# Performance work log

Hardware: AMD Instinct MI355X
Metric: run time of the kernel (lower is better)

## Reference

```python
import jax, jax.numpy as jnp
import numpy as np

CTX = 1024   # context_window
D = 512      # emb_dim
B = 8        # batch


def make_rotary_matrix(ctx, d):
    """Dense block-diagonal RoPE rotation matrices R: [ctx, d, d]."""
    pos = jnp.arange(ctx, dtype=jnp.float32)[:, None]          # [ctx, 1]
    i = jnp.arange(d // 2, dtype=jnp.float32)                  # [d/2]
    theta = pos / (10000.0 ** (2.0 * i / d))                   # [ctx, d/2]
    cos, sin = jnp.cos(theta), jnp.sin(theta)
    idx = jnp.arange(d // 2)
    R = jnp.zeros((ctx, d, d), jnp.float32)
    R = R.at[:, 2 * idx, 2 * idx].set(cos)
    R = R.at[:, 2 * idx, 2 * idx + 1].set(-sin)
    R = R.at[:, 2 * idx + 1, 2 * idx].set(sin)
    R = R.at[:, 2 * idx + 1, 2 * idx + 1].set(cos)
    return R


def setup_inputs() -> dict:
    key = jax.random.key(0)
    ks = jax.random.split(key, 8)
    s = 1.0 / np.sqrt(D)
    inp = {
        "x": jax.random.normal(ks[0], (B, CTX, D), jnp.float32),
        "w_q": jax.random.uniform(ks[1], (D, D), jnp.float32, -s, s),
        "b_q": jax.random.uniform(ks[2], (D,), jnp.float32, -s, s),
        "w_k": jax.random.uniform(ks[3], (D, D), jnp.float32, -s, s),
        "b_k": jax.random.uniform(ks[4], (D,), jnp.float32, -s, s),
        "w_v": jax.random.uniform(ks[5], (D, D), jnp.float32, -s, s),
        "b_v": jax.random.uniform(ks[6], (D,), jnp.float32, -s, s),
        "R": make_rotary_matrix(CTX, D),
        "kv_cache": 0,  # bool flag; does not affect output
    }
    return inp


def reference(x, w_q, b_q, w_k, b_k, w_v, b_v, R, kv_cache):
    B_, C, Dm = x.shape
    q = x @ w_q.T + b_q                      # [B, C, D]
    k = x @ w_k.T + b_k
    v = x @ w_v.T + b_v
    Rc = R[:C]                               # [C, D, D]
    # torch.bmm(q.transpose(0,1), R.transpose(1,2)).transpose(0,1)
    # out[b,c,e] = sum_d q[b,c,d] * R[c,e,d]
    q_rot = jnp.einsum("bcd,ced->bce", q, Rc)
    k_rot = jnp.einsum("bcd,ced->bce", k, Rc)
    # causal SDPA (eval mode: dropout omitted)
    scale = 1.0 / jnp.sqrt(jnp.asarray(Dm, jnp.float32))
    scores = jnp.einsum("bqe,bke->bqk", q_rot, k_rot) * scale   # [B, C, C]
    causal = jnp.tril(jnp.ones((C, C), bool))
    scores = jnp.where(causal, scores, jnp.finfo(scores.dtype).min)
    attn = jax.nn.softmax(scores, axis=-1)
    return jnp.einsum("bqk,bkd->bqd", attn, v)
```

## Files before the change

kernel.cpp:

```cpp
#include <hip/hip_runtime.h>

#define BATCH 8
#define CTXN  1024
#define DMODEL 512

using short8  = __attribute__((ext_vector_type(8))) short;
using f32x16  = __attribute__((ext_vector_type(16))) float;

typedef const void __attribute__((address_space(1)))* as1_cvp;
typedef void __attribute__((address_space(3)))* as3_vp;

__device__ __forceinline__ unsigned short f2bf(float f) {
  unsigned int u = __float_as_uint(f);
  u += 0x7fffu + ((u >> 16) & 1u);
  return (unsigned short)(u >> 16);
}
__device__ __forceinline__ float bf2f(unsigned short u) {
  return __uint_as_float((unsigned int)u << 16);
}

#define X4  1048576
#define W4  65536
#define CAST_BLOCKS 4864
__global__ __launch_bounds__(256) void prep_all(const float* __restrict__ x,
                                                const float* __restrict__ wq,
                                                const float* __restrict__ wk,
                                                const float* __restrict__ wv,
                                                unsigned short* __restrict__ xb,
                                                unsigned short* __restrict__ wb,
                                                float2* __restrict__ tab) {
  if (blockIdx.x < CAST_BLOCKS) {
    int gid = blockIdx.x * 256 + threadIdx.x;
    const float4* src; ushort4* dst;
    if (gid < X4)                { src = (const float4*)x  + gid;              dst = (ushort4*)xb + gid; }
    else if (gid < X4 + W4)      { int o = gid - X4;        src = (const float4*)wq + o; dst = (ushort4*)wb + o; }
    else if (gid < X4 + 2 * W4)  { int o = gid - X4 - W4;   src = (const float4*)wk + o; dst = (ushort4*)(wb + 262144) + o; }
    else                         { int o = gid - X4 - 2*W4; src = (const float4*)wv + o; dst = (ushort4*)(wb + 524288) + o; }
    float4 f = *src;
    ushort4 u;
    u.x = f2bf(f.x); u.y = f2bf(f.y); u.z = f2bf(f.z); u.w = f2bf(f.w);
    *dst = u;
  } else {
    int c = blockIdx.x - CAST_BLOCKS;
    int i = threadIdx.x;
    float freq = exp2f((float)i * (-13.287712379549449f / 256.0f));
    float th = (float)c * freq;
    float sn, cs;
    sincosf(th, &sn, &cs);
    tab[c * 256 + i] = make_float2(cs, sn);
  }
}


__device__ __forceinline__ void issue_tile(const unsigned short* __restrict__ gA, int ldA,
                                           const unsigned short* __restrict__ gB, int ldB,
                                           unsigned short* sA, unsigned short* sB,
                                           int slot, int tid) {
  unsigned short* dA = sA + (slot << 13);
  unsigned short* dB = sB + (slot << 13);
#pragma unroll
  for (int c = 0; c < 2; ++c) {
    int li  = (c << 9) + tid;
    int row = li >> 3;
    int ch  = (li & 7) ^ (row & 7);
    __builtin_amdgcn_global_load_lds((as1_cvp)(gA + (size_t)row * ldA + (ch << 3)),
                                     (as3_vp)(dA + (li << 3)), 16, 0, 0);
  }
#pragma unroll
  for (int c = 0; c < 2; ++c) {
    int li  = (c << 9) + tid;
    int row = li >> 3;
    int ch  = (li & 7) ^ (row & 7);
    __builtin_amdgcn_global_load_lds((as1_cvp)(gB + (size_t)row * ldB + (ch << 3)),
                                     (as3_vp)(dB + (li << 3)), 16, 0, 0);
  }
}

__device__ __forceinline__ void gemm_pipe(const unsigned short* __restrict__ gA, int ldA,
                                          const unsigned short* __restrict__ gB, int ldB,
                                          int nt, unsigned short* sA, unsigned short* sB,
                                          int tid, f32x16 acc[2]) {
  const int l = tid & 63, w = tid >> 6, wr = w >> 2, wc = w & 3;
  const int cl = l & 31, hi = l >> 5;
  int aoff[2][4], boff[4];
#pragma unroll
  for (int m = 0; m < 2; ++m) {
    int ra = wr * 64 + m * 32 + cl;
#pragma unroll
    for (int ks = 0; ks < 4; ++ks) {
      int kc = ks * 2 + hi;
      aoff[m][ks] = ra * 64 + ((kc ^ (ra & 7)) << 3);
    }
  }
  {
    int rb = wc * 32 + cl;
#pragma unroll
    for (int ks = 0; ks < 4; ++ks) {
      int kc = ks * 2 + hi;
      boff[ks] = rb * 64 + ((kc ^ (rb & 7)) << 3);
    }
  }
  issue_tile(gA, ldA, gB, ldB, sA, sB, 0, tid);
  issue_tile(gA + 64, ldA, gB + 64, ldB, sA, sB, 1, tid);
  asm volatile("s_waitcnt vmcnt(4)" ::: "memory");
  __builtin_amdgcn_s_barrier();
  __builtin_amdgcn_sched_barrier(0);

  for (int t = 0; t < nt; ++t) {
    const unsigned short* sAb = sA + ((t & 1) << 13);
    const unsigned short* sBb = sB + ((t & 1) << 13);
    short8 af[2][4], bfv[4];
    af[0][0] = *(const short8*)(sAb + aoff[0][0]);
    af[1][0] = *(const short8*)(sAb + aoff[1][0]);
    bfv[0]   = *(const short8*)(sBb + boff[0]);
#pragma unroll
    for (int ks = 0; ks < 3; ++ks) {
      af[0][ks + 1] = *(const short8*)(sAb + aoff[0][ks + 1]);
      af[1][ks + 1] = *(const short8*)(sAb + aoff[1][ks + 1]);
      bfv[ks + 1]   = *(const short8*)(sBb + boff[ks + 1]);
      asm volatile("s_waitcnt lgkmcnt(3)" ::: "memory");
      __builtin_amdgcn_sched_barrier(0);
      __builtin_amdgcn_s_setprio(1);
      acc[0] = __builtin_amdgcn_mfma_f32_32x32x16_bf16(af[0][ks], bfv[ks], acc[0], 0, 0, 0);
      acc[1] = __builtin_amdgcn_mfma_f32_32x32x16_bf16(af[1][ks], bfv[ks], acc[1], 0, 0, 0);
      __builtin_amdgcn_s_setprio(0);
    }
    asm volatile("s_waitcnt lgkmcnt(0)" ::: "memory");
    __builtin_amdgcn_sched_barrier(0);
    __builtin_amdgcn_s_barrier();
    if (t + 2 < nt) {
      issue_tile(gA + (size_t)(t + 2) * 64, ldA, gB + (size_t)(t + 2) * 64, ldB, sA, sB, t & 1, tid);
      asm volatile("s_waitcnt vmcnt(4)" ::: "memory");
    } else {
      asm volatile("s_waitcnt vmcnt(0)" ::: "memory");
    }
    __builtin_amdgcn_sched_barrier(0);
    __builtin_amdgcn_s_setprio(1);
    acc[0] = __builtin_amdgcn_mfma_f32_32x32x16_bf16(af[0][3], bfv[3], acc[0], 0, 0, 0);
    acc[1] = __builtin_amdgcn_mfma_f32_32x32x16_bf16(af[1][3], bfv[3], acc[1], 0, 0, 0);
    __builtin_amdgcn_s_setprio(0);
    __builtin_amdgcn_s_barrier();
    __builtin_amdgcn_sched_barrier(0);
  }
}


__global__ __launch_bounds__(512, 4) void qkv_kernel(const unsigned short* __restrict__ xb,
                                                     const unsigned short* __restrict__ wb,
                                                     const float* __restrict__ bq,
                                                     const float* __restrict__ bk,
                                                     const float* __restrict__ bv,
                                                     const float2* __restrict__ tab,
                                                     unsigned short* __restrict__ qrot,
                                                     unsigned short* __restrict__ krot,
                                                     unsigned short* __restrict__ vt) {
  __shared__ __align__(16) unsigned short sA[2 * 8192];
  __shared__ __align__(16) unsigned short sB[2 * 8192];
  int t = threadIdx.x, w = t >> 6, l = t & 63, wr = w >> 2, wc = w & 3;
  int cl = l & 31, hi = l >> 5;
  int m0 = blockIdx.x * 128, n0 = blockIdx.y * 128;
  f32x16 acc[2] = {};
  gemm_pipe(xb + (size_t)m0 * 512, 512, wb + (size_t)n0 * 512, 512, 8, sA, sB, t, acc);

  int sec = n0 >> 9;
  const float* bias = (sec == 0) ? bq : (sec == 1) ? bk : bv;
  unsigned short* qk_dst = (sec == 0) ? qrot : krot;
  int e = (n0 + wc * 32 + cl) & 511;
  float bsv = bias[e];
  if (sec < 2) {
    int i2 = e >> 1;
#pragma unroll
    for (int m = 0; m < 2; ++m) {
      int rowb = m0 + wr * 64 + m * 32 + 4 * hi;
#pragma unroll
      for (int r = 0; r < 16; ++r) {
        int mg = rowb + (r & 3) + 8 * (r >> 2);
        int cpos = mg & (CTXN - 1);
        float val  = acc[m][r] + bsv;
        float part = __shfl_xor(val, 1);
        float2 cs  = tab[cpos * 256 + i2];
        float o = (e & 1) ? fmaf(part, cs.y, val * cs.x)
                          : fmaf(-part, cs.y, val * cs.x);
        qk_dst[(size_t)mg * 512 + e] = f2bf(o);
      }
    }
  } else {
#pragma unroll
    for (int m = 0; m < 2; ++m) {
      int rowb0 = m0 + wr * 64 + m * 32 + 4 * hi;
#pragma unroll
      for (int q = 0; q < 4; ++q) {
        int rowb = rowb0 + 8 * q;
        int bidx = rowb >> 10;
        int cpos = rowb & (CTXN - 1);
        ushort4 pk;
        pk.x = f2bf(acc[m][q * 4 + 0] + bsv);
        pk.y = f2bf(acc[m][q * 4 + 1] + bsv);
        pk.z = f2bf(acc[m][q * 4 + 2] + bsv);
        pk.w = f2bf(acc[m][q * 4 + 3] + bsv);
        *(ushort4*)(vt + ((size_t)bidx * 512 + e) * 1024 + cpos) = pk;
      }
    }
  }
}

__device__ const unsigned char TRI_IT[36] = {0,1,1,2,2,2,3,3,3,3,4,4,4,4,4,5,5,5,5,5,5,
                                             6,6,6,6,6,6,6,7,7,7,7,7,7,7,7};
__device__ const unsigned char TRI_JT[36] = {0,0,1,0,1,2,0,1,2,3,0,1,2,3,4,0,1,2,3,4,5,
                                             0,1,2,3,4,5,6,0,1,2,3,4,5,6,7};

__global__ __launch_bounds__(512, 4) void scores_kernel(const unsigned short* __restrict__ qr,
                                                        const unsigned short* __restrict__ kr,
                                                        unsigned short* __restrict__ S) {
  int it = TRI_IT[blockIdx.x], jt = TRI_JT[blockIdx.x], b = blockIdx.y;
  __shared__ __align__(16) unsigned short sA[2 * 8192];
  __shared__ __align__(16) unsigned short sB[2 * 8192];
  int t = threadIdx.x, w = t >> 6, l = t & 63, wr = w >> 2, wc = w & 3;
  int cl = l & 31, hi = l >> 5;
  const unsigned short* A  = qr + ((size_t)b << 19) + (size_t)it * 128 * 512;
  const unsigned short* Bp = kr + ((size_t)b << 19) + (size_t)jt * 128 * 512;
  f32x16 acc[2] = {};
  gemm_pipe(A, 512, Bp, 512, 8, sA, sB, t, acc);

  const float scale = 0.04419417382415922f;
  unsigned short* Sb = S + ((size_t)b << 20);
  int j = jt * 128 + wc * 32 + cl;
#pragma unroll
  for (int m = 0; m < 2; ++m) {
    int iqb = it * 128 + wr * 64 + m * 32 + 4 * hi;
#pragma unroll
    for (int r = 0; r < 16; ++r)
      Sb[(size_t)(iqb + (r & 3) + 8 * (r >> 2)) * 1024 + j] = f2bf(acc[m][r] * scale);
  }
}

__global__ __launch_bounds__(256) void softmax_kernel(const unsigned short* __restrict__ S,
                                                      unsigned short* __restrict__ P) {
  int w = threadIdx.x >> 6, l = threadIdx.x & 63;
  int i = blockIdx.x * 4 + w;
  int b = blockIdx.y;
  const unsigned short* row = S + ((size_t)b << 20) + (size_t)i * 1024;
  unsigned short* prow = P + ((size_t)b << 20) + (size_t)i * 1024;
  int len  = i + 1;
  int jmax = ((i >> 7) + 1) << 7;
  float v[16];
  float mx = -3.4e38f;
#pragma unroll
  for (int c = 0; c < 2; ++c) {
    short8 raw = *(const short8*)(row + c * 512 + l * 8);
#pragma unroll
    for (int jj = 0; jj < 8; ++jj) {
      int j = c * 512 + l * 8 + jj;
      float f = bf2f((unsigned short)raw[jj]);
      v[c * 8 + jj] = (j < len) ? f : -3.4e38f;
      mx = fmaxf(mx, v[c * 8 + jj]);
    }
  }
#pragma unroll
  for (int o = 32; o > 0; o >>= 1) mx = fmaxf(mx, __shfl_xor(mx, o));
  float sm = 0.0f;
#pragma unroll
  for (int p = 0; p < 16; ++p) {
    int j = (p >> 3) * 512 + l * 8 + (p & 7);
    v[p] = (j < len) ? __expf(v[p] - mx) : 0.0f;
    sm += v[p];
  }
#pragma unroll
  for (int o = 32; o > 0; o >>= 1) sm += __shfl_xor(sm, o);
  float inv = 1.0f / sm;
#pragma unroll
  for (int c = 0; c < 2; ++c) {
    int jbase = c * 512 + l * 8;
    if (jbase < jmax) {
      short8 outv;
#pragma unroll
      for (int jj = 0; jj < 8; ++jj) outv[jj] = (short)f2bf(v[c * 8 + jj] * inv);
      *(short8*)(prow + jbase) = outv;
    }
  }
}

__global__ __launch_bounds__(512, 4) void pv_kernel(const unsigned short* __restrict__ P,
                                                    const unsigned short* __restrict__ vt,
                                                    float* __restrict__ out) {
  int it = blockIdx.x, nt2 = blockIdx.y, b = blockIdx.z;
  __shared__ __align__(16) unsigned short sA[2 * 8192];
  __shared__ __align__(16) unsigned short sB[2 * 8192];
  int t = threadIdx.x, w = t >> 6, l = t & 63, wr = w >> 2, wc = w & 3;
  int cl = l & 31, hi = l >> 5;
  const unsigned short* A  = P  + ((size_t)b << 20) + (size_t)it * 128 * 1024;
  const unsigned short* Bp = vt + ((size_t)b << 19) + (size_t)nt2 * 128 * 1024;
  int nt = (it + 1) * 2;
  f32x16 acc[2] = {};
  gemm_pipe(A, 1024, Bp, 1024, nt, sA, sB, t, acc);

  float* ob = out + ((size_t)b << 19);
  int d = nt2 * 128 + wc * 32 + cl;
#pragma unroll
  for (int m = 0; m < 2; ++m) {
    int iqb = it * 128 + wr * 64 + m * 32 + 4 * hi;
#pragma unroll
    for (int r = 0; r < 16; ++r)
      ob[(size_t)(iqb + (r & 3) + 8 * (r >> 2)) * 512 + d] = acc[m][r];
  }
}

extern "C" void kernel_launch(void* const* d_in, const int* in_sizes, int n_in,
                              void* d_out, int out_size, void* d_ws, size_t ws_size,
                              hipStream_t stream) {
  const float* x  = (const float*)d_in[0];
  const float* wq = (const float*)d_in[1];
  const float* bq = (const float*)d_in[2];
  const float* wk = (const float*)d_in[3];
  const float* bk = (const float*)d_in[4];
  const float* wv = (const float*)d_in[5];
  const float* bv = (const float*)d_in[6];
  float* out = (float*)d_out;

  char* ws = (char*)d_ws;
  float2*         tab  = (float2*)(ws);
  unsigned short* xb   = (unsigned short*)(ws + (2ull  << 20));
  unsigned short* wb   = (unsigned short*)(ws + (10ull << 20));
  unsigned short* qrot = (unsigned short*)(ws + (12ull << 20));
  unsigned short* krot = (unsigned short*)(ws + (20ull << 20));
  unsigned short* vt   = (unsigned short*)(ws + (28ull << 20));
  unsigned short* S    = (unsigned short*)(ws + (36ull << 20));
  unsigned short* P    = (unsigned short*)(ws + (52ull << 20));

  prep_all<<<dim3(CAST_BLOCKS + CTXN), dim3(256), 0, stream>>>(x, wq, wk, wv, xb, wb, tab);
  qkv_kernel<<<dim3(64, 12), dim3(512), 0, stream>>>(xb, wb, bq, bk, bv, tab, qrot, krot, vt);
  scores_kernel<<<dim3(36, BATCH), dim3(512), 0, stream>>>(qrot, krot, S);
  softmax_kernel<<<dim3(256, BATCH), dim3(256), 0, stream>>>(S, P);
  pv_kernel<<<dim3(8, 4, BATCH), dim3(512), 0, stream>>>(P, vt, out);
}
```

Baseline: 77.15 us.

## Fuse scores, softmax and PV into a single flash-attention kernel

Replaces the three-kernel attention path (scores to global S, softmax to global P, then PV GEMM) with one flash-style kernel. Each 512-thread block owns 32 query rows of one batch and walks KV tiles of 256 with an online softmax: row max and sum are reduced across waves through shared memory, and P is staged in LDS as bf16. The goal is to drop the S and P round trips through HBM and two kernel launches. In exchange it reads Q, K and V fragments straight from global memory with no LDS tiling, uses small 32-row tiles across 256 blocks with uneven causal work, and adds three barriers per KV tile.

```diff
diff --git a/kernel.cpp b/kernel.cpp
--- a/kernel.cpp
+++ b/kernel.cpp
@@ -14,9 +14,6 @@
   unsigned int u = __float_as_uint(f);
   u += 0x7fffu + ((u >> 16) & 1u);
   return (unsigned short)(u >> 16);
-}
-__device__ __forceinline__ float bf2f(unsigned short u) {
-  return __uint_as_float((unsigned int)u << 16);
 }
 
 #define X4  1048576
@@ -51,7 +48,6 @@
   }
 }
 
-
 __device__ __forceinline__ void issue_tile(const unsigned short* __restrict__ gA, int ldA,
                                            const unsigned short* __restrict__ gB, int ldB,
                                            unsigned short* sA, unsigned short* sB,
@@ -204,104 +200,113 @@
   }
 }
 
-__device__ const unsigned char TRI_IT[36] = {0,1,1,2,2,2,3,3,3,3,4,4,4,4,4,5,5,5,5,5,5,
-                                             6,6,6,6,6,6,6,7,7,7,7,7,7,7,7};
-__device__ const unsigned char TRI_JT[36] = {0,0,1,0,1,2,0,1,2,3,0,1,2,3,4,0,1,2,3,4,5,
-                                             0,1,2,3,4,5,6,0,1,2,3,4,5,6,7};
-
-__global__ __launch_bounds__(512, 4) void scores_kernel(const unsigned short* __restrict__ qr,
-                                                        const unsigned short* __restrict__ kr,
-                                                        unsigned short* __restrict__ S) {
-  int it = TRI_IT[blockIdx.x], jt = TRI_JT[blockIdx.x], b = blockIdx.y;
-  __shared__ __align__(16) unsigned short sA[2 * 8192];
-  __shared__ __align__(16) unsigned short sB[2 * 8192];
-  int t = threadIdx.x, w = t >> 6, l = t & 63, wr = w >> 2, wc = w & 3;
-  int cl = l & 31, hi = l >> 5;
-  const unsigned short* A  = qr + ((size_t)b << 19) + (size_t)it * 128 * 512;
-  const unsigned short* Bp = kr + ((size_t)b << 19) + (size_t)jt * 128 * 512;
-  f32x16 acc[2] = {};
-  gemm_pipe(A, 512, Bp, 512, 8, sA, sB, t, acc);
+#define KVB 256
+#define PPITCH 264
+
+__global__ __launch_bounds__(512, 2) void fattn_kernel(const unsigned short* __restrict__ qrot,
+                                                       const unsigned short* __restrict__ krot,
+                                                       const unsigned short* __restrict__ vt,
+                                                       float* __restrict__ out) {
+  int wgid = blockIdx.x;
+  int s = wgid >> 3, b = wgid & 7;
+  int iq0 = s * 32;
+  int kvmax = iq0 + 32;
+  int njt = (kvmax + KVB - 1) / KVB;
+
+  const unsigned short* Qb = qrot + ((size_t)b << 19) + (size_t)iq0 * 512;
+  const unsigned short* Kb = krot + ((size_t)b << 19);
+  const unsigned short* Vb = vt   + ((size_t)b << 19);
+
+  __shared__ __align__(16) unsigned short Ps[32 * PPITCH];
+  __shared__ float redM[32][8];
+  __shared__ float redS[32][8];
+
+  int t = threadIdx.x, w = t >> 6, l = t & 63, cl = l & 31, hi = l >> 5;
+
+  f32x16 O0 = {}, O1 = {};
+  float m_run[16], l_run[16];
+#pragma unroll
+  for (int rr = 0; rr < 16; ++rr) { m_run[rr] = -3.0e38f; l_run[rr] = 0.0f; }
 
   const float scale = 0.04419417382415922f;
-  unsigned short* Sb = S + ((size_t)b << 20);
-  int j = jt * 128 + wc * 32 + cl;
-#pragma unroll
-  for (int m = 0; m < 2; ++m) {
-    int iqb = it * 128 + wr * 64 + m * 32 + 4 * hi;
-#pragma unroll
-    for (int r = 0; r < 16; ++r)
-      Sb[(size_t)(iqb + (r & 3) + 8 * (r >> 2)) * 1024 + j] = f2bf(acc[m][r] * scale);
-  }
-}
-
-__global__ __launch_bounds__(256) void softmax_kernel(const unsigned short* __restrict__ S,
-                                                      unsigned short* __restrict__ P) {
-  int w = threadIdx.x >> 6, l = threadIdx.x & 63;
-  int i = blockIdx.x * 4 + w;
-  int b = blockIdx.y;
-  const unsigned short* row = S + ((size_t)b << 20) + (size_t)i * 1024;
-  unsigned short* prow = P + ((size_t)b << 20) + (size_t)i * 1024;
-  int len  = i + 1;
-  int jmax = ((i >> 7) + 1) << 7;
-  float v[16];
-  float mx = -3.4e38f;
-#pragma unroll
-  for (int c = 0; c < 2; ++c) {
-    short8 raw = *(const short8*)(row + c * 512 + l * 8);
-#pragma unroll
-    for (int jj = 0; jj < 8; ++jj) {
-      int j = c * 512 + l * 8 + jj;
-      float f = bf2f((unsigned short)raw[jj]);
-      v[c * 8 + jj] = (j < len) ? f : -3.4e38f;
-      mx = fmaxf(mx, v[c * 8 + jj]);
-    }
-  }
-#pragma unroll
-  for (int o = 32; o > 0; o >>= 1) mx = fmaxf(mx, __shfl_xor(mx, o));
-  float sm = 0.0f;
-#pragma unroll
-  for (int p = 0; p < 16; ++p) {
-    int j = (p >> 3) * 512 + l * 8 + (p & 7);
-    v[p] = (j < len) ? __expf(v[p] - mx) : 0.0f;
-    sm += v[p];
-  }
-#pragma unroll
-  for (int o = 32; o > 0; o >>= 1) sm += __shfl_xor(sm, o);
-  float inv = 1.0f / sm;
-#pragma unroll
-  for (int c = 0; c < 2; ++c) {
-    int jbase = c * 512 + l * 8;
-    if (jbase < jmax) {
-      short8 outv;
-#pragma unroll
-      for (int jj = 0; jj < 8; ++jj) outv[jj] = (short)f2bf(v[c * 8 + jj] * inv);
-      *(short8*)(prow + jbase) = outv;
-    }
-  }
-}
-
-__global__ __launch_bounds__(512, 4) void pv_kernel(const unsigned short* __restrict__ P,
-                                                    const unsigned short* __restrict__ vt,
-                                                    float* __restrict__ out) {
-  int it = blockIdx.x, nt2 = blockIdx.y, b = blockIdx.z;
-  __shared__ __align__(16) unsigned short sA[2 * 8192];
-  __shared__ __align__(16) unsigned short sB[2 * 8192];
-  int t = threadIdx.x, w = t >> 6, l = t & 63, wr = w >> 2, wc = w & 3;
-  int cl = l & 31, hi = l >> 5;
-  const unsigned short* A  = P  + ((size_t)b << 20) + (size_t)it * 128 * 1024;
-  const unsigned short* Bp = vt + ((size_t)b << 19) + (size_t)nt2 * 128 * 1024;
-  int nt = (it + 1) * 2;
-  f32x16 acc[2] = {};
-  gemm_pipe(A, 1024, Bp, 1024, nt, sA, sB, t, acc);
-
-  float* ob = out + ((size_t)b << 19);
-  int d = nt2 * 128 + wc * 32 + cl;
-#pragma unroll
-  for (int m = 0; m < 2; ++m) {
-    int iqb = it * 128 + wr * 64 + m * 32 + 4 * hi;
-#pragma unroll
-    for (int r = 0; r < 16; ++r)
-      ob[(size_t)(iqb + (r & 3) + 8 * (r >> 2)) * 512 + d] = acc[m][r];
+
+  for (int jt = 0; jt < njt; ++jt) {
+    int j0 = jt * KVB + w * 32;
+    bool act = (j0 < kvmax);
+    f32x16 aE = {}, aO = {};
+    if (act) {
+      const unsigned short* Kw = Kb + (size_t)j0 * 512;
+#pragma unroll
+      for (int ks = 0; ks < 32; ++ks) {
+        short8 qa = *(const short8*)(Qb + (size_t)cl * 512 + ks * 16 + hi * 8);
+        short8 kf = *(const short8*)(Kw + (size_t)cl * 512 + ks * 16 + hi * 8);
+        if (ks & 1) aO = __builtin_amdgcn_mfma_f32_32x32x16_bf16(qa, kf, aO, 0, 0, 0);
+        else        aE = __builtin_amdgcn_mfma_f32_32x32x16_bf16(qa, kf, aE, 0, 0, 0);
+      }
+    }
+    int jcol = j0 + cl;
+    float sv[16];
+#pragma unroll
+    for (int rr = 0; rr < 16; ++rr) {
+      int rowi = iq0 + (rr & 3) + 8 * (rr >> 2) + 4 * hi;
+      float xv = (aE[rr] + aO[rr]) * scale;
+      sv[rr] = (act && jcol <= rowi) ? xv : -3.0e38f;
+    }
+#pragma unroll
+    for (int rr = 0; rr < 16; ++rr) {
+      float m = sv[rr];
+#pragma unroll
+      for (int o = 16; o > 0; o >>= 1) m = fmaxf(m, __shfl_xor(m, o));
+      if (cl == 0) redM[(rr & 3) + 8 * (rr >> 2) + 4 * hi][w] = m;
+    }
+    __syncthreads();
+    float sc[16];
+#pragma unroll
+    for (int rr = 0; rr < 16; ++rr) {
+      int row = (rr & 3) + 8 * (rr >> 2) + 4 * hi;
+      float4 a = *(const float4*)&redM[row][0];
+      float4 bq = *(const float4*)&redM[row][4];
+      float tm = fmaxf(fmaxf(fmaxf(a.x, a.y), fmaxf(a.z, a.w)),
+                       fmaxf(fmaxf(bq.x, bq.y), fmaxf(bq.z, bq.w)));
+      float nm = fmaxf(m_run[rr], tm);
+      sc[rr] = __expf(m_run[rr] - nm);
+      m_run[rr] = nm;
+      float p = __expf(sv[rr] - nm);
+      sv[rr] = p;
+      float sp = p;
+#pragma unroll
+      for (int o = 16; o > 0; o >>= 1) sp += __shfl_xor(sp, o);
+      if (cl == 0) redS[row][w] = sp;
+      Ps[row * PPITCH + w * 32 + cl] = f2bf(p);
+      O0[rr] *= sc[rr];
+      O1[rr] *= sc[rr];
+    }
+    __syncthreads();
+#pragma unroll
+    for (int rr = 0; rr < 16; ++rr) {
+      int row = (rr & 3) + 8 * (rr >> 2) + 4 * hi;
+      float4 a = *(const float4*)&redS[row][0];
+      float4 bq = *(const float4*)&redS[row][4];
+      l_run[rr] = l_run[rr] * sc[rr] + (a.x + a.y + a.z + a.w + bq.x + bq.y + bq.z + bq.w);
+    }
+    int kkmax = min(16, (kvmax - jt * KVB + 15) >> 4);
+    const unsigned short* Vw = Vb + (size_t)(w * 64) * 1024 + jt * KVB;
+    for (int kk = 0; kk < kkmax; ++kk) {
+      short8 pa = *(const short8*)(Ps + cl * PPITCH + kk * 16 + hi * 8);
+      short8 v0 = *(const short8*)(Vw + (size_t)cl * 1024 + kk * 16 + hi * 8);
+      short8 v1 = *(const short8*)(Vw + (size_t)(cl + 32) * 1024 + kk * 16 + hi * 8);
+      O0 = __builtin_amdgcn_mfma_f32_32x32x16_bf16(pa, v0, O0, 0, 0, 0);
+      O1 = __builtin_amdgcn_mfma_f32_32x32x16_bf16(pa, v1, O1, 0, 0, 0);
+    }
+    __syncthreads();
+  }
+  float* ob = out + ((size_t)b << 19) + (size_t)iq0 * 512;
+#pragma unroll
+  for (int rr = 0; rr < 16; ++rr) {
+    int row = (rr & 3) + 8 * (rr >> 2) + 4 * hi;
+    float inv = 1.0f / l_run[rr];
+    ob[(size_t)row * 512 + w * 64 + cl]      = O0[rr] * inv;
+    ob[(size_t)row * 512 + w * 64 + 32 + cl] = O1[rr] * inv;
   }
 }
 
@@ -324,12 +329,8 @@
   unsigned short* qrot = (unsigned short*)(ws + (12ull << 20));
   unsigned short* krot = (unsigned short*)(ws + (20ull << 20));
   unsigned short* vt   = (unsigned short*)(ws + (28ull << 20));
-  unsigned short* S    = (unsigned short*)(ws + (36ull << 20));
-  unsigned short* P    = (unsigned short*)(ws + (52ull << 20));
 
   prep_all<<<dim3(CAST_BLOCKS + CTXN), dim3(256), 0, stream>>>(x, wq, wk, wv, xb, wb, tab);
   qkv_kernel<<<dim3(64, 12), dim3(512), 0, stream>>>(xb, wb, bq, bk, bv, tab, qrot, krot, vt);
-  scores_kernel<<<dim3(36, BATCH), dim3(512), 0, stream>>>(qrot, krot, S);
-  softmax_kernel<<<dim3(256, BATCH), dim3(256), 0, stream>>>(S, P);
-  pv_kernel<<<dim3(8, 4, BATCH), dim3(512), 0, stream>>>(P, vt, out);
-}
+  fattn_kernel<<<dim3(256), dim3(512), 0, stream>>>(qrot, krot, vt, out);
+}
```

Result: slower. 153.5 us (+99.0%).

## Use 64-row query tiles with 256-thread blocks for scores and PV GEMMs

Applied to the files above, without the earlier changes.

Adds a 64x128 tile GEMM pipeline (gemm_pipe64) with 4 warps and switches the scores and PV kernels to it. Causal triangle enumeration becomes finer (72 tiles per batch instead of 36), and PV blocks for 64-row query tiles stop at the 128-column boundary. The aim is more blocks for better CU occupancy and load balance, and less wasted causal work. The cost is lower per-block reuse of the B operand and more global loads per unit of work.

```diff
diff --git a/kernel.cpp b/kernel.cpp
--- a/kernel.cpp
+++ b/kernel.cpp
@@ -51,7 +51,6 @@
   }
 }
 
-
 __device__ __forceinline__ void issue_tile(const unsigned short* __restrict__ gA, int ldA,
                                            const unsigned short* __restrict__ gB, int ldB,
                                            unsigned short* sA, unsigned short* sB,
@@ -131,6 +130,98 @@
     if (t + 2 < nt) {
       issue_tile(gA + (size_t)(t + 2) * 64, ldA, gB + (size_t)(t + 2) * 64, ldB, sA, sB, t & 1, tid);
       asm volatile("s_waitcnt vmcnt(4)" ::: "memory");
+    } else {
+      asm volatile("s_waitcnt vmcnt(0)" ::: "memory");
+    }
+    __builtin_amdgcn_sched_barrier(0);
+    __builtin_amdgcn_s_setprio(1);
+    acc[0] = __builtin_amdgcn_mfma_f32_32x32x16_bf16(af[0][3], bfv[3], acc[0], 0, 0, 0);
+    acc[1] = __builtin_amdgcn_mfma_f32_32x32x16_bf16(af[1][3], bfv[3], acc[1], 0, 0, 0);
+    __builtin_amdgcn_s_setprio(0);
+    __builtin_amdgcn_s_barrier();
+    __builtin_amdgcn_sched_barrier(0);
+  }
+}
+
+__device__ __forceinline__ void issue_tile64(const unsigned short* __restrict__ gA, int ldA,
+                                             const unsigned short* __restrict__ gB, int ldB,
+                                             unsigned short* sA, unsigned short* sB,
+                                             int slot, int tid) {
+  unsigned short* dA = sA + (slot << 12);
+  unsigned short* dB = sB + (slot << 13);
+#pragma unroll
+  for (int c = 0; c < 2; ++c) {
+    int li  = (c << 8) + tid;
+    int row = li >> 3;
+    int ch  = (li & 7) ^ (row & 7);
+    __builtin_amdgcn_global_load_lds((as1_cvp)(gA + (size_t)row * ldA + (ch << 3)),
+                                     (as3_vp)(dA + (li << 3)), 16, 0, 0);
+  }
+#pragma unroll
+  for (int c = 0; c < 4; ++c) {
+    int li  = (c << 8) + tid;
+    int row = li >> 3;
+    int ch  = (li & 7) ^ (row & 7);
+    __builtin_amdgcn_global_load_lds((as1_cvp)(gB + (size_t)row * ldB + (ch << 3)),
+                                     (as3_vp)(dB + (li << 3)), 16, 0, 0);
+  }
+}
+
+__device__ __forceinline__ void gemm_pipe64(const unsigned short* __restrict__ gA, int ldA,
+                                            const unsigned short* __restrict__ gB, int ldB,
+                                            int nt, unsigned short* sA, unsigned short* sB,
+                                            int tid, f32x16 acc[2]) {
+  const int l = tid & 63, w = tid >> 6;
+  const int cl = l & 31, hi = l >> 5;
+  int aoff[2][4], boff[4];
+#pragma unroll
+  for (int m = 0; m < 2; ++m) {
+    int ra = m * 32 + cl;
+#pragma unroll
+    for (int ks = 0; ks < 4; ++ks) {
+      int kc = ks * 2 + hi;
+      aoff[m][ks] = ra * 64 + ((kc ^ (ra & 7)) << 3);
+    }
+  }
+  {
+    int rb = w * 32 + cl;
+#pragma unroll
+    for (int ks = 0; ks < 4; ++ks) {
+      int kc = ks * 2 + hi;
+      boff[ks] = rb * 64 + ((kc ^ (rb & 7)) << 3);
+    }
+  }
+  issue_tile64(gA, ldA, gB, ldB, sA, sB, 0, tid);
+  issue_tile64(gA + 64, ldA, gB + 64, ldB, sA, sB, 1, tid);
+  asm volatile("s_waitcnt vmcnt(6)" ::: "memory");
+  __builtin_amdgcn_s_barrier();
+  __builtin_amdgcn_sched_barrier(0);
+
+  for (int t = 0; t < nt; ++t) {
+    const unsigned short* sAb = sA + ((t & 1) << 12);
+    const unsigned short* sBb = sB + ((t & 1) << 13);
+    short8 af[2][4], bfv[4];
+    af[0][0] = *(const short8*)(sAb + aoff[0][0]);
+    af[1][0] = *(const short8*)(sAb + aoff[1][0]);
+    bfv[0]   = *(const short8*)(sBb + boff[0]);
+#pragma unroll
+    for (int ks = 0; ks < 3; ++ks) {
+      af[0][ks + 1] = *(const short8*)(sAb + aoff[0][ks + 1]);
+      af[1][ks + 1] = *(const short8*)(sAb + aoff[1][ks + 1]);
+      bfv[ks + 1]   = *(const short8*)(sBb + boff[ks + 1]);
+      asm volatile("s_waitcnt lgkmcnt(3)" ::: "memory");
+      __builtin_amdgcn_sched_barrier(0);
+      __builtin_amdgcn_s_setprio(1);
+      acc[0] = __builtin_amdgcn_mfma_f32_32x32x16_bf16(af[0][ks], bfv[ks], acc[0], 0, 0, 0);
+      acc[1] = __builtin_amdgcn_mfma_f32_32x32x16_bf16(af[1][ks], bfv[ks], acc[1], 0, 0, 0);
+      __builtin_amdgcn_s_setprio(0);
+    }
+    asm volatile("s_waitcnt lgkmcnt(0)" ::: "memory");
+    __builtin_amdgcn_sched_barrier(0);
+    __builtin_amdgcn_s_barrier();
+    if (t + 2 < nt) {
+      issue_tile64(gA + (size_t)(t + 2) * 64, ldA, gB + (size_t)(t + 2) * 64, ldB, sA, sB, t & 1, tid);
+      asm volatile("s_waitcnt vmcnt(6)" ::: "memory");
     } else {
       asm volatile("s_waitcnt vmcnt(0)" ::: "memory");
     }
@@ -204,30 +295,36 @@
   }
 }
 
-__device__ const unsigned char TRI_IT[36] = {0,1,1,2,2,2,3,3,3,3,4,4,4,4,4,5,5,5,5,5,5,
-                                             6,6,6,6,6,6,6,7,7,7,7,7,7,7,7};
-__device__ const unsigned char TRI_JT[36] = {0,0,1,0,1,2,0,1,2,3,0,1,2,3,4,0,1,2,3,4,5,
-                                             0,1,2,3,4,5,6,0,1,2,3,4,5,6,7};
-
-__global__ __launch_bounds__(512, 4) void scores_kernel(const unsigned short* __restrict__ qr,
+__device__ const unsigned char T64_IT[72] = {
+  0,1,2,2,3,3,4,4,4,5,5,5,6,6,6,6,7,7,7,7,
+  8,8,8,8,8,9,9,9,9,9,10,10,10,10,10,10,11,11,11,11,11,11,
+  12,12,12,12,12,12,12,13,13,13,13,13,13,13,
+  14,14,14,14,14,14,14,14,15,15,15,15,15,15,15,15};
+__device__ const unsigned char T64_JT[72] = {
+  0,0,0,1,0,1,0,1,2,0,1,2,0,1,2,3,0,1,2,3,
+  0,1,2,3,4,0,1,2,3,4,0,1,2,3,4,5,0,1,2,3,4,5,
+  0,1,2,3,4,5,6,0,1,2,3,4,5,6,
+  0,1,2,3,4,5,6,7,0,1,2,3,4,5,6,7};
+
+__global__ __launch_bounds__(256, 3) void scores_kernel(const unsigned short* __restrict__ qr,
                                                         const unsigned short* __restrict__ kr,
                                                         unsigned short* __restrict__ S) {
-  int it = TRI_IT[blockIdx.x], jt = TRI_JT[blockIdx.x], b = blockIdx.y;
-  __shared__ __align__(16) unsigned short sA[2 * 8192];
+  int it = T64_IT[blockIdx.x], jt = T64_JT[blockIdx.x], b = blockIdx.y;
+  __shared__ __align__(16) unsigned short sA[2 * 4096];
   __shared__ __align__(16) unsigned short sB[2 * 8192];
-  int t = threadIdx.x, w = t >> 6, l = t & 63, wr = w >> 2, wc = w & 3;
+  int t = threadIdx.x, w = t >> 6, l = t & 63;
   int cl = l & 31, hi = l >> 5;
-  const unsigned short* A  = qr + ((size_t)b << 19) + (size_t)it * 128 * 512;
+  const unsigned short* A  = qr + ((size_t)b << 19) + (size_t)it * 64 * 512;
   const unsigned short* Bp = kr + ((size_t)b << 19) + (size_t)jt * 128 * 512;
   f32x16 acc[2] = {};
-  gemm_pipe(A, 512, Bp, 512, 8, sA, sB, t, acc);
+  gemm_pipe64(A, 512, Bp, 512, 8, sA, sB, t, acc);
 
   const float scale = 0.04419417382415922f;
   unsigned short* Sb = S + ((size_t)b << 20);
-  int j = jt * 128 + wc * 32 + cl;
+  int j = jt * 128 + w * 32 + cl;
 #pragma unroll
   for (int m = 0; m < 2; ++m) {
-    int iqb = it * 128 + wr * 64 + m * 32 + 4 * hi;
+    int iqb = it * 64 + m * 32 + 4 * hi;
 #pragma unroll
     for (int r = 0; r < 16; ++r)
       Sb[(size_t)(iqb + (r & 3) + 8 * (r >> 2)) * 1024 + j] = f2bf(acc[m][r] * scale);
@@ -280,25 +377,25 @@
   }
 }
 
-__global__ __launch_bounds__(512, 4) void pv_kernel(const unsigned short* __restrict__ P,
+__global__ __launch_bounds__(256, 3) void pv_kernel(const unsigned short* __restrict__ P,
                                                     const unsigned short* __restrict__ vt,
                                                     float* __restrict__ out) {
   int it = blockIdx.x, nt2 = blockIdx.y, b = blockIdx.z;
-  __shared__ __align__(16) unsigned short sA[2 * 8192];
+  __shared__ __align__(16) unsigned short sA[2 * 4096];
   __shared__ __align__(16) unsigned short sB[2 * 8192];
-  int t = threadIdx.x, w = t >> 6, l = t & 63, wr = w >> 2, wc = w & 3;
+  int t = threadIdx.x, w = t >> 6, l = t & 63;
   int cl = l & 31, hi = l >> 5;
-  const unsigned short* A  = P  + ((size_t)b << 20) + (size_t)it * 128 * 1024;
+  const unsigned short* A  = P  + ((size_t)b << 20) + (size_t)it * 64 * 1024;
   const unsigned short* Bp = vt + ((size_t)b << 19) + (size_t)nt2 * 128 * 1024;
-  int nt = (it + 1) * 2;
+  int nt = ((it >> 1) + 1) * 2;
   f32x16 acc[2] = {};
-  gemm_pipe(A, 1024, Bp, 1024, nt, sA, sB, t, acc);
+  gemm_pipe64(A, 1024, Bp, 1024, nt, sA, sB, t, acc);
 
   float* ob = out + ((size_t)b << 19);
-  int d = nt2 * 128 + wc * 32 + cl;
+  int d = nt2 * 128 + w * 32 + cl;
 #pragma unroll
   for (int m = 0; m < 2; ++m) {
-    int iqb = it * 128 + wr * 64 + m * 32 + 4 * hi;
+    int iqb = it * 64 + m * 32 + 4 * hi;
 #pragma unroll
     for (int r = 0; r < 16; ++r)
       ob[(size_t)(iqb + (r & 3) + 8 * (r >> 2)) * 512 + d] = acc[m][r];
@@ -329,7 +426,7 @@
 
   prep_all<<<dim3(CAST_BLOCKS + CTXN), dim3(256), 0, stream>>>(x, wq, wk, wv, xb, wb, tab);
   qkv_kernel<<<dim3(64, 12), dim3(512), 0, stream>>>(xb, wb, bq, bk, bv, tab, qrot, krot, vt);
-  scores_kernel<<<dim3(36, BATCH), dim3(512), 0, stream>>>(qrot, krot, S);
+  scores_kernel<<<dim3(72, BATCH), dim3(256), 0, stream>>>(qrot, krot, S);
   softmax_kernel<<<dim3(256, BATCH), dim3(256), 0, stream>>>(S, P);
-  pv_kernel<<<dim3(8, 4, BATCH), dim3(512), 0, stream>>>(P, vt, out);
-}
+  pv_kernel<<<dim3(16, 4, BATCH), dim3(256), 0, stream>>>(P, vt, out);
+}
```

Result: faster. 73.88 us (-4.2%).

## Shrink GEMM tiles to 64x128 with 256-thread blocks for more parallelism

Applied to the files above, without the earlier changes.

Replaces the 128x128 GEMM tile, run by 512 threads in 8 waves, with a 64x128 tile run by 256 threads in 4 waves. The QKV, scores and PV kernels all switch to the smaller tile. The scores triangle is re-enumerated at finer granularity (72 tiles), and PV's causal K-extent is recomputed per 64-row tile. The aim is to raise block count and occupancy and to cut wasted causal work, trading away some B-tile reuse per block and adding extra loads and barriers.

```diff
diff --git a/kernel.cpp b/kernel.cpp
--- a/kernel.cpp
+++ b/kernel.cpp
@@ -51,24 +51,23 @@
   }
 }
 
-
-__device__ __forceinline__ void issue_tile(const unsigned short* __restrict__ gA, int ldA,
-                                           const unsigned short* __restrict__ gB, int ldB,
-                                           unsigned short* sA, unsigned short* sB,
-                                           int slot, int tid) {
-  unsigned short* dA = sA + (slot << 13);
+__device__ __forceinline__ void issue_tile64(const unsigned short* __restrict__ gA, int ldA,
+                                             const unsigned short* __restrict__ gB, int ldB,
+                                             unsigned short* sA, unsigned short* sB,
+                                             int slot, int tid) {
+  unsigned short* dA = sA + (slot << 12);
   unsigned short* dB = sB + (slot << 13);
 #pragma unroll
   for (int c = 0; c < 2; ++c) {
-    int li  = (c << 9) + tid;
+    int li  = (c << 8) + tid;
     int row = li >> 3;
     int ch  = (li & 7) ^ (row & 7);
     __builtin_amdgcn_global_load_lds((as1_cvp)(gA + (size_t)row * ldA + (ch << 3)),
                                      (as3_vp)(dA + (li << 3)), 16, 0, 0);
   }
 #pragma unroll
-  for (int c = 0; c < 2; ++c) {
-    int li  = (c << 9) + tid;
+  for (int c = 0; c < 4; ++c) {
+    int li  = (c << 8) + tid;
     int row = li >> 3;
     int ch  = (li & 7) ^ (row & 7);
     __builtin_amdgcn_global_load_lds((as1_cvp)(gB + (size_t)row * ldB + (ch << 3)),
@@ -76,16 +75,16 @@
   }
 }
 
-__device__ __forceinline__ void gemm_pipe(const unsigned short* __restrict__ gA, int ldA,
-                                          const unsigned short* __restrict__ gB, int ldB,
-                                          int nt, unsigned short* sA, unsigned short* sB,
-                                          int tid, f32x16 acc[2]) {
-  const int l = tid & 63, w = tid >> 6, wr = w >> 2, wc = w & 3;
+__device__ __forceinline__ void gemm_pipe64(const unsigned short* __restrict__ gA, int ldA,
+                                            const unsigned short* __restrict__ gB, int ldB,
+                                            int nt, unsigned short* sA, unsigned short* sB,
+                                            int tid, f32x16 acc[2]) {
+  const int l = tid & 63, w = tid >> 6;
   const int cl = l & 31, hi = l >> 5;
   int aoff[2][4], boff[4];
 #pragma unroll
   for (int m = 0; m < 2; ++m) {
-    int ra = wr * 64 + m * 32 + cl;
+    int ra = m * 32 + cl;
 #pragma unroll
     for (int ks = 0; ks < 4; ++ks) {
       int kc = ks * 2 + hi;
@@ -93,21 +92,21 @@
     }
   }
   {
-    int rb = wc * 32 + cl;
+    int rb = w * 32 + cl;
 #pragma unroll
     for (int ks = 0; ks < 4; ++ks) {
       int kc = ks * 2 + hi;
       boff[ks] = rb * 64 + ((kc ^ (rb & 7)) << 3);
     }
   }
-  issue_tile(gA, ldA, gB, ldB, sA, sB, 0, tid);
-  issue_tile(gA + 64, ldA, gB + 64, ldB, sA, sB, 1, tid);
-  asm volatile("s_waitcnt vmcnt(4)" ::: "memory");
+  issue_tile64(gA, ldA, gB, ldB, sA, sB, 0, tid);
+  issue_tile64(gA + 64, ldA, gB + 64, ldB, sA, sB, 1, tid);
+  asm volatile("s_waitcnt vmcnt(6)" ::: "memory");
   __builtin_amdgcn_s_barrier();
   __builtin_amdgcn_sched_barrier(0);
 
   for (int t = 0; t < nt; ++t) {
-    const unsigned short* sAb = sA + ((t & 1) << 13);
+    const unsigned short* sAb = sA + ((t & 1) << 12);
     const unsigned short* sBb = sB + ((t & 1) << 13);
     short8 af[2][4], bfv[4];
     af[0][0] = *(const short8*)(sAb + aoff[0][0]);
@@ -129,8 +128,8 @@
     __builtin_amdgcn_sched_barrier(0);
     __builtin_amdgcn_s_barrier();
     if (t + 2 < nt) {
-      issue_tile(gA + (size_t)(t + 2) * 64, ldA, gB + (size_t)(t + 2) * 64, ldB, sA, sB, t & 1, tid);
-      asm volatile("s_waitcnt vmcnt(4)" ::: "memory");
+      issue_tile64(gA + (size_t)(t + 2) * 64, ldA, gB + (size_t)(t + 2) * 64, ldB, sA, sB, t & 1, tid);
+      asm volatile("s_waitcnt vmcnt(6)" ::: "memory");
     } else {
       asm volatile("s_waitcnt vmcnt(0)" ::: "memory");
     }
@@ -145,7 +144,7 @@
 }
 
 
-__global__ __launch_bounds__(512, 4) void qkv_kernel(const unsigned short* __restrict__ xb,
+__global__ __launch_bounds__(256, 3) void qkv_kernel(const unsigned short* __restrict__ xb,
                                                      const unsigned short* __restrict__ wb,
                                                      const float* __restrict__ bq,
                                                      const float* __restrict__ bk,
@@ -154,24 +153,24 @@
                                                      unsigned short* __restrict__ qrot,
                                                      unsigned short* __restrict__ krot,
                                                      unsigned short* __restrict__ vt) {
-  __shared__ __align__(16) unsigned short sA[2 * 8192];
+  __shared__ __align__(16) unsigned short sA[2 * 4096];
   __shared__ __align__(16) unsigned short sB[2 * 8192];
-  int t = threadIdx.x, w = t >> 6, l = t & 63, wr = w >> 2, wc = w & 3;
+  int t = threadIdx.x, w = t >> 6, l = t & 63;
   int cl = l & 31, hi = l >> 5;
-  int m0 = blockIdx.x * 128, n0 = blockIdx.y * 128;
+  int m0 = blockIdx.x * 64, n0 = blockIdx.y * 128;
   f32x16 acc[2] = {};
-  gemm_pipe(xb + (size_t)m0 * 512, 512, wb + (size_t)n0 * 512, 512, 8, sA, sB, t, acc);
+  gemm_pipe64(xb + (size_t)m0 * 512, 512, wb + (size_t)n0 * 512, 512, 8, sA, sB, t, acc);
 
   int sec = n0 >> 9;
   const float* bias = (sec == 0) ? bq : (sec == 1) ? bk : bv;
   unsigned short* qk_dst = (sec == 0) ? qrot : krot;
-  int e = (n0 + wc * 32 + cl) & 511;
+  int e = (n0 + w * 32 + cl) & 511;
   float bsv = bias[e];
   if (sec < 2) {
     int i2 = e >> 1;
 #pragma unroll
     for (int m = 0; m < 2; ++m) {
-      int rowb = m0 + wr * 64 + m * 32 + 4 * hi;
+      int rowb = m0 + m * 32 + 4 * hi;
 #pragma unroll
       for (int r = 0; r < 16; ++r) {
         int mg = rowb + (r & 3) + 8 * (r >> 2);
@@ -187,7 +186,7 @@
   } else {
 #pragma unroll
     for (int m = 0; m < 2; ++m) {
-      int rowb0 = m0 + wr * 64 + m * 32 + 4 * hi;
+      int rowb0 = m0 + m * 32 + 4 * hi;
 #pragma unroll
       for (int q = 0; q < 4; ++q) {
         int rowb = rowb0 + 8 * q;
@@ -204,30 +203,36 @@
   }
 }
 
-__device__ const unsigned char TRI_IT[36] = {0,1,1,2,2,2,3,3,3,3,4,4,4,4,4,5,5,5,5,5,5,
-                                             6,6,6,6,6,6,6,7,7,7,7,7,7,7,7};
-__device__ const unsigned char TRI_JT[36] = {0,0,1,0,1,2,0,1,2,3,0,1,2,3,4,0,1,2,3,4,5,
-                                             0,1,2,3,4,5,6,0,1,2,3,4,5,6,7};
-
-__global__ __launch_bounds__(512, 4) void scores_kernel(const unsigned short* __restrict__ qr,
+__device__ const unsigned char T64_IT[72] = {
+  0,1,2,2,3,3,4,4,4,5,5,5,6,6,6,6,7,7,7,7,
+  8,8,8,8,8,9,9,9,9,9,10,10,10,10,10,10,11,11,11,11,11,11,
+  12,12,12,12,12,12,12,13,13,13,13,13,13,13,
+  14,14,14,14,14,14,14,14,15,15,15,15,15,15,15,15};
+__device__ const unsigned char T64_JT[72] = {
+  0,0,0,1,0,1,0,1,2,0,1,2,0,1,2,3,0,1,2,3,
+  0,1,2,3,4,0,1,2,3,4,0,1,2,3,4,5,0,1,2,3,4,5,
+  0,1,2,3,4,5,6,0,1,2,3,4,5,6,
+  0,1,2,3,4,5,6,7,0,1,2,3,4,5,6,7};
+
+__global__ __launch_bounds__(256, 3) void scores_kernel(const unsigned short* __restrict__ qr,
                                                         const unsigned short* __restrict__ kr,
                                                         unsigned short* __restrict__ S) {
-  int it = TRI_IT[blockIdx.x], jt = TRI_JT[blockIdx.x], b = blockIdx.y;
-  __shared__ __align__(16) unsigned short sA[2 * 8192];
+  int it = T64_IT[blockIdx.x], jt = T64_JT[blockIdx.x], b = blockIdx.y;
+  __shared__ __align__(16) unsigned short sA[2 * 4096];
   __shared__ __align__(16) unsigned short sB[2 * 8192];
-  int t = threadIdx.x, w = t >> 6, l = t & 63, wr = w >> 2, wc = w & 3;
+  int t = threadIdx.x, w = t >> 6, l = t & 63;
   int cl = l & 31, hi = l >> 5;
-  const unsigned short* A  = qr + ((size_t)b << 19) + (size_t)it * 128 * 512;
+  const unsigned short* A  = qr + ((size_t)b << 19) + (size_t)it * 64 * 512;
   const unsigned short* Bp = kr + ((size_t)b << 19) + (size_t)jt * 128 * 512;
   f32x16 acc[2] = {};
-  gemm_pipe(A, 512, Bp, 512, 8, sA, sB, t, acc);
+  gemm_pipe64(A, 512, Bp, 512, 8, sA, sB, t, acc);
 
   const float scale = 0.04419417382415922f;
   unsigned short* Sb = S + ((size_t)b << 20);
-  int j = jt * 128 + wc * 32 + cl;
+  int j = jt * 128 + w * 32 + cl;
 #pragma unroll
   for (int m = 0; m < 2; ++m) {
-    int iqb = it * 128 + wr * 64 + m * 32 + 4 * hi;
+    int iqb = it * 64 + m * 32 + 4 * hi;
 #pragma unroll
     for (int r = 0; r < 16; ++r)
       Sb[(size_t)(iqb + (r & 3) + 8 * (r >> 2)) * 1024 + j] = f2bf(acc[m][r] * scale);
@@ -280,25 +285,25 @@
   }
 }
 
-__global__ __launch_bounds__(512, 4) void pv_kernel(const unsigned short* __restrict__ P,
+__global__ __launch_bounds__(256, 3) void pv_kernel(const unsigned short* __restrict__ P,
                                                     const unsigned short* __restrict__ vt,
                                                     float* __restrict__ out) {
   int it = blockIdx.x, nt2 = blockIdx.y, b = blockIdx.z;
-  __shared__ __align__(16) unsigned short sA[2 * 8192];
+  __shared__ __align__(16) unsigned short sA[2 * 4096];
   __shared__ __align__(16) unsigned short sB[2 * 8192];
-  int t = threadIdx.x, w = t >> 6, l = t & 63, wr = w >> 2, wc = w & 3;
+  int t = threadIdx.x, w = t >> 6, l = t & 63;
   int cl = l & 31, hi = l >> 5;
-  const unsigned short* A  = P  + ((size_t)b << 20) + (size_t)it * 128 * 1024;
+  const unsigned short* A  = P  + ((size_t)b << 20) + (size_t)it * 64 * 1024;
   const unsigned short* Bp = vt + ((size_t)b << 19) + (size_t)nt2 * 128 * 1024;
-  int nt = (it + 1) * 2;
+  int nt = ((it >> 1) + 1) * 2;
   f32x16 acc[2] = {};
-  gemm_pipe(A, 1024, Bp, 1024, nt, sA, sB, t, acc);
+  gemm_pipe64(A, 1024, Bp, 1024, nt, sA, sB, t, acc);
 
   float* ob = out + ((size_t)b << 19);
-  int d = nt2 * 128 + wc * 32 + cl;
+  int d = nt2 * 128 + w * 32 + cl;
 #pragma unroll
   for (int m = 0; m < 2; ++m) {
-    int iqb = it * 128 + wr * 64 + m * 32 + 4 * hi;
+    int iqb = it * 64 + m * 32 + 4 * hi;
 #pragma unroll
     for (int r = 0; r < 16; ++r)
       ob[(size_t)(iqb + (r & 3) + 8 * (r >> 2)) * 512 + d] = acc[m][r];
@@ -328,8 +333,8 @@
   unsigned short* P    = (unsigned short*)(ws + (52ull << 20));
 
   prep_all<<<dim3(CAST_BLOCKS + CTXN), dim3(256), 0, stream>>>(x, wq, wk, wv, xb, wb, tab);
-  qkv_kernel<<<dim3(64, 12), dim3(512), 0, stream>>>(xb, wb, bq, bk, bv, tab, qrot, krot, vt);
-  scores_kernel<<<dim3(36, BATCH), dim3(512), 0, stream>>>(qrot, krot, S);
+  qkv_kernel<<<dim3(128, 12), dim3(256), 0, stream>>>(xb, wb, bq, bk, bv, tab, qrot, krot, vt);
+  scores_kernel<<<dim3(72, BATCH), dim3(256), 0, stream>>>(qrot, krot, S);
   softmax_kernel<<<dim3(256, BATCH), dim3(256), 0, stream>>>(S, P);
-  pv_kernel<<<dim3(8, 4, BATCH), dim3(512), 0, stream>>>(P, vt, out);
-}
+  pv_kernel<<<dim3(16, 4, BATCH), dim3(256), 0, stream>>>(P, vt, out);
+}
```

Result: faster. 75.08 us (-2.7%).
